# Optimization experiments

Hardware: AMD Instinct MI355X
Metric: run time of the kernel (lower is better)

The kernel has to match this reference:

```python
import jax, jax.numpy as jnp
import numpy as np
from jax.ops import segment_sum, segment_max

N_USERS = 50000
N_ITEMS = 30000
N_ENTITIES = 80000
D = 64
KG_HOPS = 2        # context_hops / KG_layers
LGCN_LAYERS = 2    # n_layers
TEMP = 0.2
N_KG_EDGES = 2_000_000
N_INTERACT = 1_000_000
N_ADJ = 2_000_000
EPS_PD = 1e-6      # torch PairwiseDistance default eps


def _normalize(x):
    # F.normalize(x, p=2, dim=-1)
    n = jnp.linalg.norm(x, axis=-1, keepdims=True)
    return x / jnp.clip(n, 1e-12)


def _spmm(rows, cols, vals, x, n_rows):
    # sparse (n_rows x k) @ dense (k x d) via gather + segment_sum
    return segment_sum(vals[:, None] * x[cols], rows, num_segments=n_rows)


def setup_inputs() -> dict:
    key = jax.random.key(0)
    ks = jax.random.split(key, 9)
    all_embed = jax.random.normal(ks[0], (N_USERS + N_ENTITIES, D), dtype=jnp.float32) * 0.1
    interact_vals = jax.random.uniform(ks[1], (N_INTERACT,), dtype=jnp.float32)
    adj_vals = jax.random.uniform(ks[2], (N_ADJ,), dtype=jnp.float32)
    edge_index = jax.random.randint(ks[3], (2, N_KG_EDGES), 0, N_ENTITIES, dtype=jnp.int32)
    edge_type = jax.random.randint(ks[4], (N_KG_EDGES,), 0, 32, dtype=jnp.int32)
    interact_rows = jnp.sort(jax.random.randint(ks[5], (N_INTERACT,), 0, N_USERS, dtype=jnp.int32))
    interact_cols = jax.random.randint(ks[6], (N_INTERACT,), 0, N_ITEMS, dtype=jnp.int32)
    adj_rows = jax.random.randint(ks[7], (N_ADJ,), 0, N_USERS + N_ITEMS, dtype=jnp.int32)
    adj_cols = jax.random.randint(ks[8], (N_ADJ,), 0, N_USERS + N_ITEMS, dtype=jnp.int32)
    return {
        "all_embed": all_embed,
        "interact_vals": interact_vals,
        "adj_vals": adj_vals,
        "edge_index": edge_index,
        "edge_type": edge_type,
        "interact_rows": interact_rows,
        "interact_cols": interact_cols,
        "adj_rows": adj_rows,
        "adj_cols": adj_cols,
    }


def _forward(all_embed, interact_vals, adj_vals, edge_index, interact_rows,
             interact_cols, adj_rows, adj_cols):
    user_emb = all_embed[:N_USERS]
    entity_emb = all_embed[N_USERS:]
    head, tail = edge_index[0], edge_index[1]

    u_res, e_res = user_emb, entity_emb
    u, e = user_emb, entity_emb
    ones = jnp.ones((head.shape[0],), dtype=entity_emb.dtype)
    cnt = jnp.clip(segment_sum(ones, head, num_segments=N_ENTITIES), 1.0)

    for _ in range(KG_HOPS):
        # scatter_mean KG aggregation: entity_agg[h] = mean over tails of edges with head h
        entity_agg = segment_sum(e[tail], head, num_segments=N_ENTITIES) / cnt[:, None]
        item_agg = entity_agg[:N_ITEMS]
        # user_mean = interact_map @ entity_agg[:n_items]
        user_mean = _spmm(interact_rows, interact_cols, interact_vals, item_agg, N_USERS)
        # pairwise L2 distance per interaction nnz
        diff = item_agg[interact_cols] - user_mean[interact_rows] + EPS_PD
        score = jnp.linalg.norm(diff, axis=-1) / TEMP
        # sparse softmax over rows (users)
        m = segment_max(score, interact_rows, num_segments=N_USERS)
        ex = jnp.exp(score - m[interact_rows])
        denom = segment_sum(ex, interact_rows, num_segments=N_USERS)
        att = ex / denom[interact_rows]
        # user_agg = sparse.mm(soft_score_mat, item_agg)
        user_agg = segment_sum(att[:, None] * item_agg[interact_cols],
                               interact_rows, num_segments=N_USERS)
        e = _normalize(entity_agg)
        u = _normalize(user_agg)
        e_res = e_res + e
        u_res = u_res + u

    # LightGCN over bipartite graph
    x = jnp.concatenate([u_res, e_res[:N_ITEMS]], axis=0)  # [n_users+n_items, D]
    acc = x
    for _ in range(LGCN_LAYERS):
        x = _spmm(adj_rows, adj_cols, adj_vals, x, N_USERS + N_ITEMS)
        acc = acc + x
    out = acc / float(LGCN_LAYERS + 1)
    return out[:N_USERS], out[N_USERS:]


def reference(all_embed, interact_vals, adj_vals, edge_index, edge_type,
              interact_rows, interact_cols, adj_rows, adj_cols):
    # edge_type is passed through the original forward but unused by Aggregator
    return _forward(all_embed, interact_vals, adj_vals, edge_index,
                    interact_rows, interact_cols, adj_rows, adj_cols)
```

## Files before the change

kernel.cpp:

```cpp
#include <hip/hip_runtime.h>
#include <math.h>

#define N_USERS 50000
#define N_ITEMS 30000
#define N_ENTITIES 80000
#define N_UI (N_USERS + N_ITEMS)
#define D 64
#define N_KG_EDGES 2000000
#define N_INTERACT 1000000
#define N_ADJ 2000000
#define INV_TEMP 5.0f
#define EPS_PD 1e-6f
#define SHIFT 7
#define NB 625
#define BKEYS 128
#define BMASK 127
#define EPB 8192
#define BIG 1024
#define GRID_EP 245
#define UH_GRID 12500
#define KG2_GRID 7500
#define CVT_GRID 1875

typedef _Float16 f16;

__device__ __forceinline__ float4 ld_h4(const f16* p) {
    struct h4 { f16 x, y, z, w; };
    h4 h = *(const h4*)p;
    return make_float4((float)h.x, (float)h.y, (float)h.z, (float)h.w);
}

__device__ __forceinline__ void st_h4(f16* p, float4 v) {
    struct h4 { f16 x, y, z, w; };
    h4 h = {(f16)v.x, (f16)v.y, (f16)v.z, (f16)v.w};
    *(h4*)p = h;
}

__global__ void bhist_plus(const int* __restrict__ kg_ei, const int* __restrict__ adj_r,
                           const int* __restrict__ irows, int* __restrict__ bcntK,
                           int* __restrict__ bcntA, int* __restrict__ rowstart) {
    __shared__ int h[NB];
    int bb = blockIdx.x;
    if (bb < 2 * GRID_EP) {
        bool kg = bb < GRID_EP;
        const int* keys = kg ? kg_ei : adj_r;
        int* bcnt = kg ? bcntK : bcntA;
        int blk = kg ? bb : bb - GRID_EP;
        int n = kg ? N_KG_EDGES : N_ADJ;
        for (int i = threadIdx.x; i < NB; i += BIG) h[i] = 0;
        __syncthreads();
        int e0 = blk * EPB, e1 = min(e0 + EPB, n);
        for (int e = e0 + (int)threadIdx.x; e < e1; e += BIG)
            atomicAdd(&h[keys[e] >> SHIFT], 1);
        __syncthreads();
        for (int i = threadIdx.x; i < NB; i += BIG)
            if (h[i]) atomicAdd(&bcnt[i], h[i]);
    } else {
        int r = (bb - 2 * GRID_EP) * BIG + threadIdx.x;
        if (r > N_USERS) return;
        int lo = 0, hi = N_INTERACT;
        while (lo < hi) {
            int mid = (lo + hi) >> 1;
            if (irows[mid] < r) lo = mid + 1; else hi = mid;
        }
        rowstart[r] = lo;
    }
}

__global__ void bscan_both(const int* __restrict__ cntK, int* __restrict__ boffK,
                           int* __restrict__ bcurK, const int* __restrict__ cntA,
                           int* __restrict__ boffA, int* __restrict__ bcurA) {
    __shared__ int wp[4];
    __shared__ int carry_s;
    const int* cnt = blockIdx.x ? cntA : cntK;
    int* boff = blockIdx.x ? boffA : boffK;
    int* bcur = blockIdx.x ? bcurA : bcurK;
    int lane = threadIdx.x & 63, wv = threadIdx.x >> 6;
    if (threadIdx.x == 0) { carry_s = 0; boff[0] = 0; }
    __syncthreads();
    for (int base = 0; base < NB; base += 256) {
        int i = base + (int)threadIdx.x;
        int v = (i < NB) ? cnt[i] : 0;
        int x = v;
        #pragma unroll
        for (int o = 1; o < 64; o <<= 1) {
            int t = __shfl_up(x, o, 64);
            if (lane >= o) x += t;
        }
        if (lane == 63) wp[wv] = x;
        __syncthreads();
        int add = carry_s;
        for (int j = 0; j < wv; ++j) add += wp[j];
        int incl = x + add;
        if (i < NB) { boff[i + 1] = incl; bcur[i] = incl - v; }
        __syncthreads();
        if (threadIdx.x == 255) carry_s = incl;
        __syncthreads();
    }
}

__global__ void binA_both(const int* __restrict__ kg_ei, int* __restrict__ bcurK,
                          int* __restrict__ kg_bin, const int* __restrict__ adj_r,
                          const int* __restrict__ adj_c, const float* __restrict__ adj_v,
                          int* __restrict__ bcurA, int2* __restrict__ rc) {
    __shared__ int hist[NB], base[NB];
    bool kg = blockIdx.x < GRID_EP;
    int blk = kg ? blockIdx.x : blockIdx.x - GRID_EP;
    int n = kg ? N_KG_EDGES : N_ADJ;
    int* bcur = kg ? bcurK : bcurA;
    const int* keys = kg ? kg_ei : adj_r;
    for (int i = threadIdx.x; i < NB; i += BIG) hist[i] = 0;
    __syncthreads();
    int e0 = blk * EPB;
    for (int i = threadIdx.x; i < EPB; i += BIG) {
        int e = e0 + i;
        if (e < n) atomicAdd(&hist[keys[e] >> SHIFT], 1);
    }
    __syncthreads();
    for (int b = threadIdx.x; b < NB; b += BIG)
        base[b] = hist[b] ? atomicAdd(&bcur[b], hist[b]) : 0;
    __syncthreads();
    for (int i = threadIdx.x; i < NB; i += BIG) hist[i] = 0;
    __syncthreads();
    for (int i = threadIdx.x; i < EPB; i += BIG) {
        int e = e0 + i;
        if (e >= n) continue;
        int k = keys[e];
        int b = k >> SHIFT;
        int slot = base[b] + atomicAdd(&hist[b], 1);
        if (kg) kg_bin[slot] = (kg_ei[n + e] << SHIFT) | (k & BMASK);
        else    rc[slot] = make_int2((adj_c[e] << SHIFT) | (k & BMASK),
                                     __float_as_int(adj_v[e]));
    }
}

__global__ void binC_both(const int* __restrict__ boffK, const int* __restrict__ kg_bin,
                          int* __restrict__ tails, int* __restrict__ rowptrK,
                          float* __restrict__ icnt, const int* __restrict__ boffA,
                          const int2* __restrict__ rc, int2* __restrict__ pair,
                          int* __restrict__ rowptrA) {
    __shared__ int cnt_s[BKEYS];
    __shared__ int cur_s[BKEYS];
    __shared__ int wp2[2];
    bool kg = blockIdx.x < NB;
    int b = kg ? blockIdx.x : blockIdx.x - NB;
    const int* boff = kg ? boffK : boffA;
    int k0 = b << SHIFT;
    int s = boff[b], t = boff[b + 1];
    if (threadIdx.x < BKEYS) cnt_s[threadIdx.x] = 0;
    __syncthreads();
    for (int i = s + (int)threadIdx.x; i < t; i += 256)
        atomicAdd(&cnt_s[(kg ? kg_bin[i] : rc[i].x) & BMASK], 1);
    __syncthreads();
    int lane = threadIdx.x & 63, wv = threadIdx.x >> 6;
    int v = (threadIdx.x < BKEYS) ? cnt_s[threadIdx.x] : 0;
    int x = v;
    #pragma unroll
    for (int o = 1; o < 64; o <<= 1) {
        int tt = __shfl_up(x, o, 64);
        if (lane >= o) x += tt;
    }
    if (threadIdx.x < BKEYS && lane == 63) wp2[wv] = x;
    __syncthreads();
    int add = (wv == 1) ? wp2[0] : 0;
    int excl = s + (x - v) + add;
    if (threadIdx.x < BKEYS) {
        cur_s[threadIdx.x] = excl;
        if (kg) {
            rowptrK[k0 + threadIdx.x] = excl;
            icnt[k0 + threadIdx.x] = 1.0f / fmaxf((float)v, 1.0f);
        } else {
            rowptrA[k0 + threadIdx.x] = excl;
        }
    }
    if (threadIdx.x == 0 && b == NB - 1) {
        if (kg) rowptrK[N_ENTITIES] = t; else rowptrA[N_UI] = t;
    }
    __syncthreads();
    if (kg) {
        for (int i = s + (int)threadIdx.x; i < t; i += 256) {
            int p = kg_bin[i];
            int slot = atomicAdd(&cur_s[p & BMASK], 1);
            tails[slot] = (unsigned)p >> SHIFT;
        }
    } else {
        for (int i = s + (int)threadIdx.x; i < t; i += 256) {
            int2 p = rc[i];
            int slot = atomicAdd(&cur_s[p.x & BMASK], 1);
            pair[slot] = make_int2((unsigned)p.x >> SHIFT, p.y);
        }
    }
}

template <bool FIRST>
__device__ __forceinline__ void kg_hop_body(
        int wid, const int* __restrict__ rowptr, const int* __restrict__ tails,
        const float* __restrict__ icnt, const float* __restrict__ Ain,
        float* __restrict__ Aout, float* __restrict__ ER,
        const float* __restrict__ ERI, float* __restrict__ snorm, int nrows) {
    int lane = threadIdx.x & 63;
    int g = lane >> 4, gl = lane & 15;
    if (wid >= nrows) return;
    int s = rowptr[wid], t = rowptr[wid + 1];
    float4 acc = {0.f, 0.f, 0.f, 0.f};
    for (int e = s + g; e < t; e += 16) {
        int e1 = e + 4, e2 = e + 8, e3 = e + 12;
        int c0 = tails[e];
        int c1 = (e1 < t) ? tails[e1] : 0;
        int c2 = (e2 < t) ? tails[e2] : 0;
        int c3 = (e3 < t) ? tails[e3] : 0;
        float4 r0 = *(const float4*)(Ain + (size_t)c0 * D + gl * 4);
        float4 r1 = {0.f, 0.f, 0.f, 0.f};
        float4 r2 = {0.f, 0.f, 0.f, 0.f};
        float4 r3 = {0.f, 0.f, 0.f, 0.f};
        if (e1 < t) r1 = *(const float4*)(Ain + (size_t)c1 * D + gl * 4);
        if (e2 < t) r2 = *(const float4*)(Ain + (size_t)c2 * D + gl * 4);
        if (e3 < t) r3 = *(const float4*)(Ain + (size_t)c3 * D + gl * 4);
        acc.x += (r0.x + r1.x) + (r2.x + r3.x);
        acc.y += (r0.y + r1.y) + (r2.y + r3.y);
        acc.z += (r0.z + r1.z) + (r2.z + r3.z);
        acc.w += (r0.w + r1.w) + (r2.w + r3.w);
    }
    acc.x += __shfl_xor(acc.x, 16, 64); acc.x += __shfl_xor(acc.x, 32, 64);
    acc.y += __shfl_xor(acc.y, 16, 64); acc.y += __shfl_xor(acc.y, 32, 64);
    acc.z += __shfl_xor(acc.z, 16, 64); acc.z += __shfl_xor(acc.z, 32, 64);
    acc.w += __shfl_xor(acc.w, 16, 64); acc.w += __shfl_xor(acc.w, 32, 64);
    float ss = acc.x * acc.x + acc.y * acc.y + acc.z * acc.z + acc.w * acc.w;
    ss += __shfl_xor(ss, 1, 64); ss += __shfl_xor(ss, 2, 64);
    ss += __shfl_xor(ss, 4, 64); ss += __shfl_xor(ss, 8, 64);
    float nrm = fmaxf(sqrtf(ss), 1e-12f);
    float inv = 1.0f / nrm;
    if (g == 0) {
        size_t o = (size_t)wid * D + gl * 4;
        float4 ev = {acc.x * inv, acc.y * inv, acc.z * inv, acc.w * inv};
        *(float4*)(Aout + o) = ev;
        if (wid < N_ITEMS) {
            float4 er = FIRST ? *(const float4*)(ERI + o) : *(const float4*)(ER + o);
            er.x += ev.x; er.y += ev.y; er.z += ev.z; er.w += ev.w;
            *(float4*)(ER + o) = er;
            if (gl == 0) snorm[wid] = nrm * icnt[wid];
        }
    }
}

template <bool FIRST>
__device__ __forceinline__ void user_hop_body(
        int wid, const float* __restrict__ E, const float* __restrict__ snorm,
        const int* __restrict__ rowstart, const int* __restrict__ cols,
        const float* __restrict__ vals, float* __restrict__ UR,
        const float* __restrict__ URI, f16* __restrict__ XHu) {
    int lane = threadIdx.x & 63;
    int g = lane >> 4, gl = lane & 15;
    if (wid >= N_USERS) return;
    int s = rowstart[wid], t = rowstart[wid + 1];

    float4 mean = {0.f, 0.f, 0.f, 0.f};
    #define UH_LOAD(K)                                                          \
        const int eP##K = s + g + 4 * K;                                        \
        const bool ok##K = eP##K < t;                                           \
        const int cP##K = ok##K ? cols[eP##K] : 0;                              \
        const float snP##K = ok##K ? snorm[cP##K] : 0.f;                        \
        const float vP##K = ok##K ? vals[eP##K] : 0.f;                          \
        float4 rP##K = {0.f, 0.f, 0.f, 0.f};                                    \
        if (ok##K) rP##K = *(const float4*)(E + (size_t)cP##K * D + gl * 4);
    UH_LOAD(0) UH_LOAD(1) UH_LOAD(2) UH_LOAD(3) UH_LOAD(4) UH_LOAD(5)
    #undef UH_LOAD
    #define UH_MEAN(K) {                                                        \
        float w = vP##K * snP##K;                                               \
        mean.x += w * rP##K.x; mean.y += w * rP##K.y;                           \
        mean.z += w * rP##K.z; mean.w += w * rP##K.w; }
    UH_MEAN(0) UH_MEAN(1) UH_MEAN(2) UH_MEAN(3) UH_MEAN(4) UH_MEAN(5)
    #undef UH_MEAN
    for (int e = s + g + 24; e < t; e += 4) {
        int c = cols[e];
        float w = vals[e] * snorm[c];
        float4 r = *(const float4*)(E + (size_t)c * D + gl * 4);
        mean.x += w * r.x; mean.y += w * r.y;
        mean.z += w * r.z; mean.w += w * r.w;
    }
    mean.x += __shfl_xor(mean.x, 16, 64); mean.x += __shfl_xor(mean.x, 32, 64);
    mean.y += __shfl_xor(mean.y, 16, 64); mean.y += __shfl_xor(mean.y, 32, 64);
    mean.z += __shfl_xor(mean.z, 16, 64); mean.z += __shfl_xor(mean.z, 32, 64);
    mean.w += __shfl_xor(mean.w, 16, 64); mean.w += __shfl_xor(mean.w, 32, 64);

    float m = -INFINITY, denom = 0.f;
    float4 acc = {0.f, 0.f, 0.f, 0.f};
    #define UH_SM(K) if (ok##K) {                                               \
        float4 il = {snP##K * rP##K.x, snP##K * rP##K.y,                        \
                     snP##K * rP##K.z, snP##K * rP##K.w};                       \
        float dx = il.x - mean.x + EPS_PD;                                      \
        float dy = il.y - mean.y + EPS_PD;                                      \
        float dz = il.z - mean.z + EPS_PD;                                      \
        float dw = il.w - mean.w + EPS_PD;                                      \
        float ssl = dx * dx + dy * dy + dz * dz + dw * dw;                      \
        ssl += __shfl_xor(ssl, 1, 64); ssl += __shfl_xor(ssl, 2, 64);           \
        ssl += __shfl_xor(ssl, 4, 64); ssl += __shfl_xor(ssl, 8, 64);           \
        float sc = sqrtf(ssl) * INV_TEMP;                                       \
        float m_new = fmaxf(m, sc);                                             \
        float scale = __expf(m - m_new);                                        \
        float ex = __expf(sc - m_new);                                          \
        denom = denom * scale + ex;                                             \
        acc.x = acc.x * scale + ex * il.x;                                      \
        acc.y = acc.y * scale + ex * il.y;                                      \
        acc.z = acc.z * scale + ex * il.z;                                      \
        acc.w = acc.w * scale + ex * il.w;                                      \
        m = m_new; }
    UH_SM(0) UH_SM(1) UH_SM(2) UH_SM(3) UH_SM(4) UH_SM(5)
    #undef UH_SM
    for (int e = s + g + 24; e < t; e += 4) {
        int c = cols[e];
        float sn = snorm[c];
        float4 r = *(const float4*)(E + (size_t)c * D + gl * 4);
        float4 il = {sn * r.x, sn * r.y, sn * r.z, sn * r.w};
        float dx = il.x - mean.x + EPS_PD;
        float dy = il.y - mean.y + EPS_PD;
        float dz = il.z - mean.z + EPS_PD;
        float dw = il.w - mean.w + EPS_PD;
        float ssl = dx * dx + dy * dy + dz * dz + dw * dw;
        ssl += __shfl_xor(ssl, 1, 64); ssl += __shfl_xor(ssl, 2, 64);
        ssl += __shfl_xor(ssl, 4, 64); ssl += __shfl_xor(ssl, 8, 64);
        float sc = sqrtf(ssl) * INV_TEMP;
        float m_new = fmaxf(m, sc);
        float scale = __expf(m - m_new);
        float ex = __expf(sc - m_new);
        denom = denom * scale + ex;
        acc.x = acc.x * scale + ex * il.x;
        acc.y = acc.y * scale + ex * il.y;
        acc.z = acc.z * scale + ex * il.z;
        acc.w = acc.w * scale + ex * il.w;
        m = m_new;
    }
    float mg = fmaxf(m, __shfl_xor(m, 16, 64));
    mg = fmaxf(mg, __shfl_xor(mg, 32, 64));
    float scl = __expf(fmaxf(m - mg, -88.0f));
    denom *= scl;
    acc.x *= scl; acc.y *= scl; acc.z *= scl; acc.w *= scl;
    denom += __shfl_xor(denom, 16, 64); denom += __shfl_xor(denom, 32, 64);
    acc.x += __shfl_xor(acc.x, 16, 64); acc.x += __shfl_xor(acc.x, 32, 64);
    acc.y += __shfl_xor(acc.y, 16, 64); acc.y += __shfl_xor(acc.y, 32, 64);
    acc.z += __shfl_xor(acc.z, 16, 64); acc.z += __shfl_xor(acc.z, 32, 64);
    acc.w += __shfl_xor(acc.w, 16, 64); acc.w += __shfl_xor(acc.w, 32, 64);
    float invd = denom > 0.f ? 1.0f / denom : 0.f;
    acc.x *= invd; acc.y *= invd; acc.z *= invd; acc.w *= invd;
    float ss = acc.x * acc.x + acc.y * acc.y + acc.z * acc.z + acc.w * acc.w;
    ss += __shfl_xor(ss, 1, 64); ss += __shfl_xor(ss, 2, 64);
    ss += __shfl_xor(ss, 4, 64); ss += __shfl_xor(ss, 8, 64);
    float inv = 1.0f / fmaxf(sqrtf(ss), 1e-12f);
    if (g == 0) {
        size_t o = (size_t)wid * D + gl * 4;
        float4 u = FIRST ? *(const float4*)(URI + o) : *(const float4*)(UR + o);
        u.x += acc.x * inv; u.y += acc.y * inv; u.z += acc.z * inv; u.w += acc.w * inv;
        *(float4*)(UR + o) = u;
        if (XHu) st_h4(XHu + o, u);
    }
}

__global__ void kg1_kernel(const int* __restrict__ rowptr, const int* __restrict__ tails,
                           const float* __restrict__ icnt, const float* __restrict__ Ain,
                           float* __restrict__ A1, float* __restrict__ ER,
                           const float* __restrict__ ERI, float* __restrict__ sn1) {
    int wid = (blockIdx.x * blockDim.x + threadIdx.x) >> 6;
    kg_hop_body<true>(wid, rowptr, tails, icnt, Ain, A1, ER, ERI, sn1, N_ENTITIES);
}

__global__ void mid_kernel(const float* __restrict__ A1, const float* __restrict__ sn1,
                           const int* __restrict__ rowstart, const int* __restrict__ cols,
                           const float* __restrict__ vals, float* __restrict__ UR,
                           const float* __restrict__ URI, const int* __restrict__ rowptr,
                           const int* __restrict__ tails, const float* __restrict__ icnt,
                           float* __restrict__ A0I, float* __restrict__ ER,
                           float* __restrict__ sn2) {
    if (blockIdx.x < UH_GRID) {
        int wid = (blockIdx.x * blockDim.x + threadIdx.x) >> 6;
        user_hop_body<true>(wid, A1, sn1, rowstart, cols, vals, UR, URI, nullptr);
    } else {
        int wid = (((blockIdx.x - UH_GRID) * blockDim.x) + threadIdx.x) >> 6;
        kg_hop_body<false>(wid, rowptr, tails, icnt, A1, A0I, ER, nullptr, sn2, N_ITEMS);
    }
}

__global__ void fin_kernel(const float* __restrict__ A0I, const float* __restrict__ sn2,
                           const int* __restrict__ rowstart, const int* __restrict__ cols,
                           const float* __restrict__ vals, float* __restrict__ UR,
                           f16* __restrict__ XH, const float* __restrict__ ER) {
    if (blockIdx.x < UH_GRID) {
        int wid = (blockIdx.x * blockDim.x + threadIdx.x) >> 6;
        user_hop_body<false>(wid, A0I, sn2, rowstart, cols, vals, UR, nullptr, XH);
    } else {
        int i = (blockIdx.x - UH_GRID) * blockDim.x + threadIdx.x;
        if (i < (N_ITEMS * D) / 4)
            st_h4(XH + (size_t)N_USERS * D + (size_t)i * 4,
                  *(const float4*)(ER + (size_t)i * 4));
    }
}

__device__ __forceinline__ const float* xrow32(const float* U, const float* I, int c) {
    return (c < N_USERS) ? (U + (size_t)c * D) : (I + (size_t)(c - N_USERS) * D);
}

template <int MODE>
__global__ void adj_spmm(const int* __restrict__ rowptr, const int2* __restrict__ pair,
                         const f16* __restrict__ X, const float* __restrict__ XAU,
                         const float* __restrict__ XAI, f16* __restrict__ Y,
                         float* __restrict__ out) {
    int wid = (blockIdx.x * blockDim.x + threadIdx.x) >> 6;
    int lane = threadIdx.x & 63;
    int g = lane >> 4, gl = lane & 15;
    if (wid >= N_UI) return;
    int s = rowptr[wid], t = rowptr[wid + 1];
    float4 acc = {0.f, 0.f, 0.f, 0.f};
    for (int e = s + g; e < t; e += 16) {
        int e1 = e + 4, e2 = e + 8, e3 = e + 12;
        int2 p0 = pair[e];
        int2 p1 = (e1 < t) ? pair[e1] : make_int2(0, 0);
        int2 p2 = (e2 < t) ? pair[e2] : make_int2(0, 0);
        int2 p3 = (e3 < t) ? pair[e3] : make_int2(0, 0);
        float4 r0 = ld_h4(X + (size_t)p0.x * D + gl * 4);
        float4 r1 = {0.f, 0.f, 0.f, 0.f};
        float4 r2 = {0.f, 0.f, 0.f, 0.f};
        float4 r3 = {0.f, 0.f, 0.f, 0.f};
        if (e1 < t) r1 = ld_h4(X + (size_t)p1.x * D + gl * 4);
        if (e2 < t) r2 = ld_h4(X + (size_t)p2.x * D + gl * 4);
        if (e3 < t) r3 = ld_h4(X + (size_t)p3.x * D + gl * 4);
        float v0 = __int_as_float(p0.y), v1 = __int_as_float(p1.y);
        float v2 = __int_as_float(p2.y), v3 = __int_as_float(p3.y);
        acc.x += (v0 * r0.x + v1 * r1.x) + (v2 * r2.x + v3 * r3.x);
        acc.y += (v0 * r0.y + v1 * r1.y) + (v2 * r2.y + v3 * r3.y);
        acc.z += (v0 * r0.z + v1 * r1.z) + (v2 * r2.z + v3 * r3.z);
        acc.w += (v0 * r0.w + v1 * r1.w) + (v2 * r2.w + v3 * r3.w);
    }
    acc.x += __shfl_xor(acc.x, 16, 64); acc.x += __shfl_xor(acc.x, 32, 64);
    acc.y += __shfl_xor(acc.y, 16, 64); acc.y += __shfl_xor(acc.y, 32, 64);
    acc.z += __shfl_xor(acc.z, 16, 64); acc.z += __shfl_xor(acc.z, 32, 64);
    acc.w += __shfl_xor(acc.w, 16, 64); acc.w += __shfl_xor(acc.w, 32, 64);
    if (g == 0) {
        size_t o = (size_t)wid * D + gl * 4;
        if (MODE == 0) {
            st_h4(Y + o, acc);
            const float4 xa = *(const float4*)(xrow32(XAU, XAI, wid) + gl * 4);
            float4 ov = {xa.x + acc.x, xa.y + acc.y, xa.z + acc.z, xa.w + acc.w};
            *(float4*)(out + o) = ov;
        } else {
            float4 ov = *(const float4*)(out + o);
            ov.x = (ov.x + acc.x) * (1.0f / 3.0f);
            ov.y = (ov.y + acc.y) * (1.0f / 3.0f);
            ov.z = (ov.z + acc.z) * (1.0f / 3.0f);
            ov.w = (ov.w + acc.w) * (1.0f / 3.0f);
            *(float4*)(out + o) = ov;
        }
    }
}

extern "C" void kernel_launch(void* const* d_in, const int* in_sizes, int n_in,
                              void* d_out, int out_size, void* d_ws, size_t ws_size,
                              hipStream_t stream) {
    const float* all_embed     = (const float*)d_in[0];
    const float* interact_vals = (const float*)d_in[1];
    const float* adj_vals      = (const float*)d_in[2];
    const int*   edge_index    = (const int*)d_in[3];
    const int*   interact_rows = (const int*)d_in[5];
    const int*   interact_cols = (const int*)d_in[6];
    const int*   adj_rows      = (const int*)d_in[7];
    const int*   adj_cols      = (const int*)d_in[8];
    float* out = (float*)d_out;

    const size_t usrN = (size_t)N_USERS * D;
    const size_t itmN = (size_t)N_ITEMS * D;
    const size_t entN = (size_t)N_ENTITIES * D;

    float* cur = (float*)d_ws;
    float* UR  = cur; cur += usrN;
    float* ER  = cur; cur += itmN;
    float* A0I = cur; cur += itmN;
    float* A1  = cur; cur += entN;
    int* KG_TAIL = (int*)cur; cur += N_KG_EDGES;
    int2* ADJ_PAIR = (int2*)cur; cur += 2 * (size_t)N_ADJ;
    float* ICNT   = cur; cur += N_ENTITIES;
    float* SNORM1 = cur; cur += N_ITEMS + 16;
    float* SNORM2 = cur; cur += N_ITEMS + 16;
    int* KG_ROWPTR  = (int*)cur;
    int* ADJ_ROWPTR = KG_ROWPTR + N_ENTITIES + 2;
    int* BCNT_K     = ADJ_ROWPTR + N_UI + 2;
    int* BCNT_A     = BCNT_K + NB;
    int* BOFF_K     = BCNT_A + NB;
    int* BOFF_A     = BOFF_K + NB + 1;
    int* BCUR_K     = BOFF_A + NB + 1;
    int* BCUR_A     = BCUR_K + NB;
    int* ROWSTART   = BCUR_A + NB;

    int*  KG_BIN = (int*)UR;
    int2* ADJ_RC = (int2*)A1;
    f16*  XH  = (f16*)A1;
    f16*  X1H = XH + (size_t)N_UI * D;

    hipMemsetAsync(BCNT_K, 0, 2 * NB * sizeof(int), stream);
    bhist_plus<<<2 * GRID_EP + 49, BIG, 0, stream>>>(edge_index, adj_rows, interact_rows,
                                                     BCNT_K, BCNT_A, ROWSTART);
    bscan_both<<<2, 256, 0, stream>>>(BCNT_K, BOFF_K, BCUR_K, BCNT_A, BOFF_A, BCUR_A);
    binA_both<<<2 * GRID_EP, BIG, 0, stream>>>(edge_index, BCUR_K, KG_BIN, adj_rows,
                                               adj_cols, adj_vals, BCUR_A, ADJ_RC);
    binC_both<<<2 * NB, 256, 0, stream>>>(BOFF_K, KG_BIN, KG_TAIL, KG_ROWPTR, ICNT,
                                          BOFF_A, ADJ_RC, ADJ_PAIR, ADJ_ROWPTR);

    kg1_kernel<<<N_ENTITIES / 4, 256, 0, stream>>>(KG_ROWPTR, KG_TAIL, ICNT,
                                                   all_embed + usrN, A1, ER,
                                                   all_embed + usrN, SNORM1);
    mid_kernel<<<UH_GRID + KG2_GRID, 256, 0, stream>>>(A1, SNORM1, ROWSTART,
                                                       interact_cols, interact_vals,
                                                       UR, all_embed, KG_ROWPTR, KG_TAIL,
                                                       ICNT, A0I, ER, SNORM2);
    fin_kernel<<<UH_GRID + CVT_GRID, 256, 0, stream>>>(A0I, SNORM2, ROWSTART,
                                                       interact_cols, interact_vals,
                                                       UR, XH, ER);

    adj_spmm<0><<<N_UI / 4, 256, 0, stream>>>(ADJ_ROWPTR, ADJ_PAIR, XH, UR, ER, X1H, out);
    adj_spmm<1><<<N_UI / 4, 256, 0, stream>>>(ADJ_ROWPTR, ADJ_PAIR, X1H, nullptr, nullptr,
                                              nullptr, out);
}
```

Baseline: 415.2 us.

## Pack adjacency col and fp16 value into one int; expand distance algebraically

The adjacency CSR entries now store the column index in the upper bits and the value as a 15-bit fp16 (sign dropped) in the lower bits of one 32-bit word. This halves the per-edge index traffic in the LightGCN SpMM and in the build pass. The user-attention loop expands ||sn*r - mean + eps||^2 as sn^2 - 2*sn*(r·b) + |b|^2, which avoids forming the scaled item vector and replaces the two exps of the online softmax with one. The costs are reduced precision on the adjacency values and possible cancellation error in the expanded distance. The packing also relies on column indices fitting in 17 bits and on values being nonnegative.

```diff
diff --git a/kernel.cpp b/kernel.cpp
--- a/kernel.cpp
+++ b/kernel.cpp
@@ -23,6 +23,7 @@
 #define CVT_GRID 1875
 
 typedef _Float16 f16;
+typedef unsigned short u16;
 
 __device__ __forceinline__ float4 ld_h4(const f16* p) {
     struct h4 { f16 x, y, z, w; };
@@ -36,9 +37,18 @@
     *(h4*)p = h;
 }
 
-__global__ void bhist_plus(const int* __restrict__ kg_ei, const int* __restrict__ adj_r,
-                           const int* __restrict__ irows, int* __restrict__ bcntK,
-                           int* __restrict__ bcntA, int* __restrict__ rowstart) {
+__device__ __forceinline__ u16 f16_bits(float v) {
+    f16 h = (f16)v;
+    return __builtin_bit_cast(u16, h);
+}
+
+__device__ __forceinline__ float bits_f16(unsigned b) {
+    return (float)__builtin_bit_cast(f16, (u16)b);
+}
+
+__global__ void stageA(const int* __restrict__ kg_ei, const int* __restrict__ adj_r,
+                       const int* __restrict__ irows, int* __restrict__ bcntK,
+                       int* __restrict__ bcntA, int* __restrict__ rowstart) {
     __shared__ int h[NB];
     int bb = blockIdx.x;
     if (bb < 2 * GRID_EP) {
@@ -137,7 +147,7 @@
 __global__ void binC_both(const int* __restrict__ boffK, const int* __restrict__ kg_bin,
                           int* __restrict__ tails, int* __restrict__ rowptrK,
                           float* __restrict__ icnt, const int* __restrict__ boffA,
-                          const int2* __restrict__ rc, int2* __restrict__ pair,
+                          const int2* __restrict__ rc, int* __restrict__ pair,
                           int* __restrict__ rowptrA) {
     __shared__ int cnt_s[BKEYS];
     __shared__ int cur_s[BKEYS];
@@ -187,7 +197,9 @@
         for (int i = s + (int)threadIdx.x; i < t; i += 256) {
             int2 p = rc[i];
             int slot = atomicAdd(&cur_s[p.x & BMASK], 1);
-            pair[slot] = make_int2((unsigned)p.x >> SHIFT, p.y);
+            unsigned col = (unsigned)p.x >> SHIFT;
+            unsigned vb = f16_bits(__int_as_float(p.y)) & 0x7FFFu;
+            pair[slot] = (int)((col << 15) | vb);
         }
     }
 }
@@ -283,52 +295,54 @@
     mean.z += __shfl_xor(mean.z, 16, 64); mean.z += __shfl_xor(mean.z, 32, 64);
     mean.w += __shfl_xor(mean.w, 16, 64); mean.w += __shfl_xor(mean.w, 32, 64);
 
+    float4 b = {mean.x - EPS_PD, mean.y - EPS_PD, mean.z - EPS_PD, mean.w - EPS_PD};
+    float bb = b.x * b.x + b.y * b.y + b.z * b.z + b.w * b.w;
+    bb += __shfl_xor(bb, 1, 64); bb += __shfl_xor(bb, 2, 64);
+    bb += __shfl_xor(bb, 4, 64); bb += __shfl_xor(bb, 8, 64);
+
     float m = -INFINITY, denom = 0.f;
     float4 acc = {0.f, 0.f, 0.f, 0.f};
     #define UH_SM(K) if (ok##K) {                                               \
-        float4 il = {snP##K * rP##K.x, snP##K * rP##K.y,                        \
-                     snP##K * rP##K.z, snP##K * rP##K.w};                       \
-        float dx = il.x - mean.x + EPS_PD;                                      \
-        float dy = il.y - mean.y + EPS_PD;                                      \
-        float dz = il.z - mean.z + EPS_PD;                                      \
-        float dw = il.w - mean.w + EPS_PD;                                      \
-        float ssl = dx * dx + dy * dy + dz * dz + dw * dw;                      \
-        ssl += __shfl_xor(ssl, 1, 64); ssl += __shfl_xor(ssl, 2, 64);           \
-        ssl += __shfl_xor(ssl, 4, 64); ssl += __shfl_xor(ssl, 8, 64);           \
-        float sc = sqrtf(ssl) * INV_TEMP;                                       \
-        float m_new = fmaxf(m, sc);                                             \
-        float scale = __expf(m - m_new);                                        \
-        float ex = __expf(sc - m_new);                                          \
+        float dl = rP##K.x * b.x + rP##K.y * b.y + rP##K.z * b.z + rP##K.w * b.w; \
+        dl += __shfl_xor(dl, 1, 64); dl += __shfl_xor(dl, 2, 64);               \
+        dl += __shfl_xor(dl, 4, 64); dl += __shfl_xor(dl, 8, 64);               \
+        float s2 = fmaxf(snP##K * snP##K - 2.f * snP##K * dl + bb, 0.f);        \
+        float sc = sqrtf(s2) * INV_TEMP;                                        \
+        float dlt = sc - m;                                                     \
+        float tt = __expf(fminf(dlt, -dlt));                                    \
+        bool up = dlt > 0.f;                                                    \
+        float scale = up ? tt : 1.f;                                            \
+        float ex = up ? 1.f : tt;                                               \
+        if (up) m = sc;                                                         \
         denom = denom * scale + ex;                                             \
-        acc.x = acc.x * scale + ex * il.x;                                      \
-        acc.y = acc.y * scale + ex * il.y;                                      \
-        acc.z = acc.z * scale + ex * il.z;                                      \
-        acc.w = acc.w * scale + ex * il.w;                                      \
-        m = m_new; }
+        float w = ex * snP##K;                                                  \
+        acc.x = acc.x * scale + w * rP##K.x;                                    \
+        acc.y = acc.y * scale + w * rP##K.y;                                    \
+        acc.z = acc.z * scale + w * rP##K.z;                                    \
+        acc.w = acc.w * scale + w * rP##K.w; }
     UH_SM(0) UH_SM(1) UH_SM(2) UH_SM(3) UH_SM(4) UH_SM(5)
     #undef UH_SM
     for (int e = s + g + 24; e < t; e += 4) {
         int c = cols[e];
         float sn = snorm[c];
         float4 r = *(const float4*)(E + (size_t)c * D + gl * 4);
-        float4 il = {sn * r.x, sn * r.y, sn * r.z, sn * r.w};
-        float dx = il.x - mean.x + EPS_PD;
-        float dy = il.y - mean.y + EPS_PD;
-        float dz = il.z - mean.z + EPS_PD;
-        float dw = il.w - mean.w + EPS_PD;
-        float ssl = dx * dx + dy * dy + dz * dz + dw * dw;
-        ssl += __shfl_xor(ssl, 1, 64); ssl += __shfl_xor(ssl, 2, 64);
-        ssl += __shfl_xor(ssl, 4, 64); ssl += __shfl_xor(ssl, 8, 64);
-        float sc = sqrtf(ssl) * INV_TEMP;
-        float m_new = fmaxf(m, sc);
-        float scale = __expf(m - m_new);
-        float ex = __expf(sc - m_new);
+        float dl = r.x * b.x + r.y * b.y + r.z * b.z + r.w * b.w;
+        dl += __shfl_xor(dl, 1, 64); dl += __shfl_xor(dl, 2, 64);
+        dl += __shfl_xor(dl, 4, 64); dl += __shfl_xor(dl, 8, 64);
+        float s2 = fmaxf(sn * sn - 2.f * sn * dl + bb, 0.f);
+        float sc = sqrtf(s2) * INV_TEMP;
+        float dlt = sc - m;
+        float tt = __expf(fminf(dlt, -dlt));
+        bool up = dlt > 0.f;
+        float scale = up ? tt : 1.f;
+        float ex = up ? 1.f : tt;
+        if (up) m = sc;
         denom = denom * scale + ex;
-        acc.x = acc.x * scale + ex * il.x;
-        acc.y = acc.y * scale + ex * il.y;
-        acc.z = acc.z * scale + ex * il.z;
-        acc.w = acc.w * scale + ex * il.w;
-        m = m_new;
+        float w = ex * sn;
+        acc.x = acc.x * scale + w * r.x;
+        acc.y = acc.y * scale + w * r.y;
+        acc.z = acc.z * scale + w * r.z;
+        acc.w = acc.w * scale + w * r.w;
     }
     float mg = fmaxf(m, __shfl_xor(m, 16, 64));
     mg = fmaxf(mg, __shfl_xor(mg, 32, 64));
@@ -399,7 +413,7 @@
 }
 
 template <int MODE>
-__global__ void adj_spmm(const int* __restrict__ rowptr, const int2* __restrict__ pair,
+__global__ void adj_spmm(const int* __restrict__ rowptr, const int* __restrict__ pair,
                          const f16* __restrict__ X, const float* __restrict__ XAU,
                          const float* __restrict__ XAI, f16* __restrict__ Y,
                          float* __restrict__ out) {
@@ -411,19 +425,19 @@
     float4 acc = {0.f, 0.f, 0.f, 0.f};
     for (int e = s + g; e < t; e += 16) {
         int e1 = e + 4, e2 = e + 8, e3 = e + 12;
-        int2 p0 = pair[e];
-        int2 p1 = (e1 < t) ? pair[e1] : make_int2(0, 0);
-        int2 p2 = (e2 < t) ? pair[e2] : make_int2(0, 0);
-        int2 p3 = (e3 < t) ? pair[e3] : make_int2(0, 0);
-        float4 r0 = ld_h4(X + (size_t)p0.x * D + gl * 4);
+        int p0 = pair[e];
+        int p1 = (e1 < t) ? pair[e1] : 0;
+        int p2 = (e2 < t) ? pair[e2] : 0;
+        int p3 = (e3 < t) ? pair[e3] : 0;
+        float4 r0 = ld_h4(X + (size_t)((unsigned)p0 >> 15) * D + gl * 4);
         float4 r1 = {0.f, 0.f, 0.f, 0.f};
         float4 r2 = {0.f, 0.f, 0.f, 0.f};
         float4 r3 = {0.f, 0.f, 0.f, 0.f};
-        if (e1 < t) r1 = ld_h4(X + (size_t)p1.x * D + gl * 4);
-        if (e2 < t) r2 = ld_h4(X + (size_t)p2.x * D + gl * 4);
-        if (e3 < t) r3 = ld_h4(X + (size_t)p3.x * D + gl * 4);
-        float v0 = __int_as_float(p0.y), v1 = __int_as_float(p1.y);
-        float v2 = __int_as_float(p2.y), v3 = __int_as_float(p3.y);
+        if (e1 < t) r1 = ld_h4(X + (size_t)((unsigned)p1 >> 15) * D + gl * 4);
+        if (e2 < t) r2 = ld_h4(X + (size_t)((unsigned)p2 >> 15) * D + gl * 4);
+        if (e3 < t) r3 = ld_h4(X + (size_t)((unsigned)p3 >> 15) * D + gl * 4);
+        float v0 = bits_f16(p0 & 0x7FFF), v1 = bits_f16(p1 & 0x7FFF);
+        float v2 = bits_f16(p2 & 0x7FFF), v3 = bits_f16(p3 & 0x7FFF);
         acc.x += (v0 * r0.x + v1 * r1.x) + (v2 * r2.x + v3 * r3.x);
         acc.y += (v0 * r0.y + v1 * r1.y) + (v2 * r2.y + v3 * r3.y);
         acc.z += (v0 * r0.z + v1 * r1.z) + (v2 * r2.z + v3 * r3.z);
@@ -473,8 +487,8 @@
     float* ER  = cur; cur += itmN;
     float* A0I = cur; cur += itmN;
     float* A1  = cur; cur += entN;
-    int* KG_TAIL = (int*)cur; cur += N_KG_EDGES;
-    int2* ADJ_PAIR = (int2*)cur; cur += 2 * (size_t)N_ADJ;
+    int*  KG_TAIL  = (int*)cur; cur += N_KG_EDGES;
+    int*  ADJ_PAIR = (int*)cur; cur += N_ADJ;
     float* ICNT   = cur; cur += N_ENTITIES;
     float* SNORM1 = cur; cur += N_ITEMS + 16;
     float* SNORM2 = cur; cur += N_ITEMS + 16;
@@ -494,8 +508,8 @@
     f16*  X1H = XH + (size_t)N_UI * D;
 
     hipMemsetAsync(BCNT_K, 0, 2 * NB * sizeof(int), stream);
-    bhist_plus<<<2 * GRID_EP + 49, BIG, 0, stream>>>(edge_index, adj_rows, interact_rows,
-                                                     BCNT_K, BCNT_A, ROWSTART);
+    stageA<<<2 * GRID_EP + 49, BIG, 0, stream>>>(edge_index, adj_rows, interact_rows,
+                                                 BCNT_K, BCNT_A, ROWSTART);
     bscan_both<<<2, 256, 0, stream>>>(BCNT_K, BOFF_K, BCUR_K, BCNT_A, BOFF_A, BCUR_A);
     binA_both<<<2 * GRID_EP, BIG, 0, stream>>>(edge_index, BCUR_K, KG_BIN, adj_rows,
                                                adj_cols, adj_vals, BCUR_A, ADJ_RC);
```

After: 388.6 us. 1.07x faster.
